# Optimization experiments

Hardware: AMD Instinct MI355X
Metric: run time of the kernel (lower is better)

Reference implementation:

```python
import jax, jax.numpy as jnp
import numpy as np

N_NODES = 50000
N_EDGES = 800000
NUM_FEATURES = 128
HIDDEN = 128
EMBED = 64
OUT_DIM = 1


def setup_inputs() -> dict:
    key = jax.random.key(0)
    ks = jax.random.split(key, 12)
    x = jax.random.normal(ks[0], (N_NODES, NUM_FEATURES), dtype=jnp.float32)
    edge_index = jax.random.randint(ks[1], (2, N_EDGES), 0, N_NODES, dtype=jnp.int64)

    def glorot(k, fan_in, fan_out):
        s = jnp.sqrt(6.0 / (fan_in + fan_out)).astype(jnp.float32)
        return jax.random.uniform(k, (fan_in, fan_out), jnp.float32, -s, s)

    return {
        "x": x,
        "edge_index": edge_index,
        "W1": glorot(ks[2], NUM_FEATURES, HIDDEN),
        "b1": jnp.zeros((HIDDEN,), jnp.float32),
        "Wh": glorot(ks[3], HIDDEN, HIDDEN),
        "bh": jnp.zeros((HIDDEN,), jnp.float32),
        "W2": glorot(ks[4], HIDDEN, EMBED),
        "b2": jnp.zeros((EMBED,), jnp.float32),
        "Wout": glorot(ks[5], EMBED, OUT_DIM),
        "bout": jnp.zeros((OUT_DIM,), jnp.float32),
    }


def _gcn_norm(edge_index, num_nodes):
    # Add self-loops, compute symmetric normalization deg^{-1/2} A_hat deg^{-1/2}
    loop = jnp.arange(num_nodes, dtype=edge_index.dtype)
    src = jnp.concatenate([edge_index[0], loop])
    dst = jnp.concatenate([edge_index[1], loop])
    deg = jax.ops.segment_sum(jnp.ones_like(dst, dtype=jnp.float32), dst,
                              num_segments=num_nodes)
    dis = jnp.where(deg > 0, jax.lax.rsqrt(jnp.maximum(deg, 1.0)), 0.0)
    norm = dis[src] * dis[dst]  # [E+N]
    return src, dst, norm


def _gcn_conv(h, W, b, src, dst, norm, num_nodes):
    h = h @ W  # linear transform first (PyG GCNConv)
    msg = h[src] * norm[:, None]  # gather + scale
    return jax.ops.segment_sum(msg, dst, num_segments=num_nodes) + b


def reference(x, edge_index, W1, b1, Wh, bh, W2, b2, Wout, bout):
    n = x.shape[0]
    src, dst, norm = _gcn_norm(edge_index, n)
    h = jax.nn.relu(_gcn_conv(x, W1, b1, src, dst, norm, n))  # dropout p=0 -> identity
    h = jax.nn.relu(_gcn_conv(h, Wh, bh, src, dst, norm, n))
    h = _gcn_conv(h, W2, b2, src, dst, norm, n)
    out = h @ Wout + bout
    return (out, h)
```

## Files before the change

### kernel.cpp

```cpp
#include <hip/hip_runtime.h>
#include <hip/hip_bf16.h>


#define N_NODES 50000
#define N_EDGES 800000
#define NBUCK 196
#define GB 196
#define EPB 4096

typedef __attribute__((ext_vector_type(8))) short short8;
typedef __attribute__((ext_vector_type(4))) float f32x4;

static __device__ __forceinline__ unsigned short f2bf(float f) {
    __hip_bfloat16 h = __float2bfloat16(f);
    return *reinterpret_cast<unsigned short*>(&h);
}
static __device__ __forceinline__ float bf2f(unsigned short u) {
    return __uint_as_float(((unsigned)u) << 16);
}


__global__ __launch_bounds__(256) void hist_kernel(const int* __restrict__ dstv,
                                                   int* __restrict__ H, int nE) {
    __shared__ int h[NBUCK];
    for (int i = threadIdx.x; i < NBUCK; i += 256) h[i] = 0;
    __syncthreads();
    int base = blockIdx.x * EPB;
#pragma unroll
    for (int i = 0; i < EPB / 256; ++i) {
        int e = base + i * 256 + threadIdx.x;
        if (e < nE) atomicAdd(&h[dstv[e] >> 8], 1);
    }
    __syncthreads();
    for (int i = threadIdx.x; i < NBUCK; i += 256)
        H[i * GB + blockIdx.x] = h[i];
}

__global__ __launch_bounds__(256) void scan1_kernel(int* __restrict__ H,
                                                    int* __restrict__ bsum) {
    __shared__ int s[256];
    int t = threadIdx.x;
    int k = blockIdx.x;
    int v = (t < GB) ? H[k * GB + t] : 0;
    s[t] = v;
    __syncthreads();
    for (int off = 1; off < 256; off <<= 1) {
        int u = (t >= off) ? s[t - off] : 0;
        __syncthreads();
        s[t] += u;
        __syncthreads();
    }
    if (t < GB) H[k * GB + t] = s[t] - v;
    if (t == 255) bsum[k] = s[255];
}

__global__ __launch_bounds__(256) void scan2_kernel(const int* __restrict__ bsum,
                                                    int* __restrict__ bstart,
                                                    int* __restrict__ rowoff_last) {
    __shared__ int s[256];
    int t = threadIdx.x;
    int v = (t < NBUCK) ? bsum[t] : 0;
    s[t] = v;
    __syncthreads();
    for (int off = 1; off < 256; off <<= 1) {
        int u = (t >= off) ? s[t - off] : 0;
        __syncthreads();
        s[t] += u;
        __syncthreads();
    }
    if (t < NBUCK) bstart[t] = s[t] - v;
    if (t == 0) {
        bstart[NBUCK] = N_EDGES;
        *rowoff_last = N_EDGES;
    }
}

__global__ __launch_bounds__(256) void partition_kernel(const int* __restrict__ srcv,
                                                        const int* __restrict__ dstv,
                                                        const int* __restrict__ H,
                                                        const int* __restrict__ bstart,
                                                        unsigned int* __restrict__ P, int nE) {
    __shared__ int cur[NBUCK];
    for (int i = threadIdx.x; i < NBUCK; i += 256)
        cur[i] = bstart[i] + H[i * GB + blockIdx.x];
    __syncthreads();
    int base = blockIdx.x * EPB;
#pragma unroll
    for (int i = 0; i < EPB / 256; ++i) {
        int e = base + i * 256 + threadIdx.x;
        if (e < nE) {
            int d = dstv[e];
            unsigned int pk = (unsigned int)srcv[e] | ((unsigned int)(d & 255) << 16);
            int pos = atomicAdd(&cur[d >> 8], 1);
            P[pos] = pk;
        }
    }
}

__global__ __launch_bounds__(256) void bucket_csr_kernel(const unsigned int* __restrict__ P,
                                                         const int* __restrict__ bstart,
                                                         int* __restrict__ rowoff,
                                                         float* __restrict__ dis,
                                                         int* __restrict__ csr_src, int n) {
    __shared__ int cnt[256];
    __shared__ int s[256];
    __shared__ int cur[256];
    int t = threadIdx.x;
    int k = blockIdx.x;
    int ebeg = bstart[k], eend = bstart[k + 1];
    cnt[t] = 0;
    __syncthreads();
    for (int e = ebeg + t; e < eend; e += 256)
        atomicAdd(&cnt[(P[e] >> 16) & 255], 1);
    __syncthreads();
    int myc = cnt[t];
    s[t] = myc;
    __syncthreads();
    for (int off = 1; off < 256; off <<= 1) {
        int v = (t >= off) ? s[t - off] : 0;
        __syncthreads();
        s[t] += v;
        __syncthreads();
    }
    int excl = s[t] - myc;
    int node = (k << 8) + t;
    if (node < n) {
        rowoff[node] = ebeg + excl;
        dis[node] = rsqrtf((float)(myc + 1));
    }
    cur[t] = ebeg + excl;
    __syncthreads();
    for (int e = ebeg + t; e < eend; e += 256) {
        unsigned int p = P[e];
        int pos = atomicAdd(&cur[(p >> 16) & 255], 1);
        csr_src[pos] = (int)(p & 0xFFFFu);
    }
}

__global__ __launch_bounds__(256) void wprep_all_kernel(
    const float* __restrict__ W1, const float* __restrict__ Wh, const float* __restrict__ W2,
    unsigned short* __restrict__ W1hi, unsigned short* __restrict__ W1lo,
    unsigned short* __restrict__ Whhi, unsigned short* __restrict__ Whlo,
    unsigned short* __restrict__ W2hi, unsigned short* __restrict__ W2lo) {
    int t = blockIdx.x * 256 + threadIdx.x;
    const float* W;
    unsigned short *Hi, *Lo;
    int nout, lt;
    if (t < 16384)      { W = W1; Hi = W1hi; Lo = W1lo; nout = 128; lt = t; }
    else if (t < 32768) { W = Wh; Hi = Whhi; Lo = Whlo; nout = 128; lt = t - 16384; }
    else if (t < 40960) { W = W2; Hi = W2hi; Lo = W2lo; nout = 64;  lt = t - 32768; }
    else return;
    int col = lt % nout, k = lt / nout;
    float v = W[lt];
    unsigned short hi = f2bf(v);
    unsigned short lo = f2bf(v - bf2f(hi));
    Hi[(size_t)col * 128 + k] = hi;
    Lo[(size_t)col * 128 + k] = lo;
}

template <int NOUT>
__global__ __launch_bounds__(256) void gemm_mfma_kernel(
    const float* __restrict__ A,
    const unsigned short* __restrict__ Wthi,
    const unsigned short* __restrict__ Wtlo,
    const float* __restrict__ scale,
    unsigned short* __restrict__ C, int M) {
    constexpr int LDK = 136;
    __shared__ unsigned short sAhi[64 * LDK];
    __shared__ unsigned short sAlo[64 * LDK];

    int tid = threadIdx.x;
    int w = tid >> 6, lane = tid & 63;
    int quad = lane >> 4, m = lane & 15;
    int Rbase = blockIdx.x * 64;
    int Cbase = blockIdx.y * 64;
    int r0 = (w & 1) * 32, c0 = (w >> 1) * 32;

    short8 bh[4][2], bl[4][2];
#pragma unroll
    for (int ks = 0; ks < 4; ++ks)
#pragma unroll
        for (int g = 0; g < 2; ++g) {
            size_t off = (size_t)(Cbase + c0 + g * 16 + m) * 128 + ks * 32 + quad * 8;
            bh[ks][g] = *(const short8*)(Wthi + off);
            bl[ks][g] = *(const short8*)(Wtlo + off);
        }

    for (int i = tid; i < 64 * 32; i += 256) {
        int r = i >> 5, c4 = i & 31;
        int row = Rbase + r;
        float4 v = make_float4(0.f, 0.f, 0.f, 0.f);
        if (row < M) v = ((const float4*)(A + (size_t)row * 128))[c4];
        ushort4 hi, lo;
        hi.x = f2bf(v.x); lo.x = f2bf(v.x - bf2f(hi.x));
        hi.y = f2bf(v.y); lo.y = f2bf(v.y - bf2f(hi.y));
        hi.z = f2bf(v.z); lo.z = f2bf(v.z - bf2f(hi.z));
        hi.w = f2bf(v.w); lo.w = f2bf(v.w - bf2f(hi.w));
        *(ushort4*)(sAhi + r * LDK + c4 * 4) = hi;
        *(ushort4*)(sAlo + r * LDK + c4 * 4) = lo;
    }
    __syncthreads();

    f32x4 z = {0.f, 0.f, 0.f, 0.f};
    f32x4 acc00 = z, acc01 = z, acc10 = z, acc11 = z;

#pragma unroll
    for (int ks = 0; ks < 4; ++ks) {
        int kof = ks * 32 + quad * 8;
        short8 ah0 = *(const short8*)(sAhi + (r0 + m) * LDK + kof);
        short8 ah1 = *(const short8*)(sAhi + (r0 + 16 + m) * LDK + kof);
        short8 al0 = *(const short8*)(sAlo + (r0 + m) * LDK + kof);
        short8 al1 = *(const short8*)(sAlo + (r0 + 16 + m) * LDK + kof);
        acc00 = __builtin_amdgcn_mfma_f32_16x16x32_bf16(ah0, bh[ks][0], acc00, 0, 0, 0);
        acc01 = __builtin_amdgcn_mfma_f32_16x16x32_bf16(ah0, bh[ks][1], acc01, 0, 0, 0);
        acc10 = __builtin_amdgcn_mfma_f32_16x16x32_bf16(ah1, bh[ks][0], acc10, 0, 0, 0);
        acc11 = __builtin_amdgcn_mfma_f32_16x16x32_bf16(ah1, bh[ks][1], acc11, 0, 0, 0);
        acc00 = __builtin_amdgcn_mfma_f32_16x16x32_bf16(ah0, bl[ks][0], acc00, 0, 0, 0);
        acc01 = __builtin_amdgcn_mfma_f32_16x16x32_bf16(ah0, bl[ks][1], acc01, 0, 0, 0);
        acc10 = __builtin_amdgcn_mfma_f32_16x16x32_bf16(ah1, bl[ks][0], acc10, 0, 0, 0);
        acc11 = __builtin_amdgcn_mfma_f32_16x16x32_bf16(ah1, bl[ks][1], acc11, 0, 0, 0);
        acc00 = __builtin_amdgcn_mfma_f32_16x16x32_bf16(al0, bh[ks][0], acc00, 0, 0, 0);
        acc01 = __builtin_amdgcn_mfma_f32_16x16x32_bf16(al0, bh[ks][1], acc01, 0, 0, 0);
        acc10 = __builtin_amdgcn_mfma_f32_16x16x32_bf16(al1, bh[ks][0], acc10, 0, 0, 0);
        acc11 = __builtin_amdgcn_mfma_f32_16x16x32_bf16(al1, bh[ks][1], acc11, 0, 0, 0);
    }

#pragma unroll
    for (int reg = 0; reg < 4; ++reg) {
        int row0g = Rbase + r0 + quad * 4 + reg;
        if (row0g < M) {
            float sc = scale[row0g];
            C[(size_t)row0g * NOUT + Cbase + c0 + m]      = f2bf(acc00[reg] * sc);
            C[(size_t)row0g * NOUT + Cbase + c0 + 16 + m] = f2bf(acc01[reg] * sc);
        }
        int row1g = row0g + 16;
        if (row1g < M) {
            float sc = scale[row1g];
            C[(size_t)row1g * NOUT + Cbase + c0 + m]      = f2bf(acc10[reg] * sc);
            C[(size_t)row1g * NOUT + Cbase + c0 + 16 + m] = f2bf(acc11[reg] * sc);
        }
    }
}

__global__ __launch_bounds__(256) void aggregate128_kernel(
    const int* __restrict__ rowoff, const int* __restrict__ csr_src,
    const float* __restrict__ dis, const unsigned short* __restrict__ tp,
    const float* __restrict__ bias, float* __restrict__ hout, int n) {
    int wid = (blockIdx.x * 256 + threadIdx.x) >> 6;
    int lane = threadIdx.x & 63;
    int h = lane >> 5, lc = lane & 31;
    int n0 = wid * 2;
    if (n0 >= n) return;
    int n1 = n0 + 1;
    bool has1 = (n1 < n);

    float a0[4] = {0.f, 0.f, 0.f, 0.f};
    float a1[4] = {0.f, 0.f, 0.f, 0.f};

#define ROW128(node) (*((const ushort4*)(tp + (size_t)(node) * 128) + lc))
#define ACC(a, u) { a[0] += bf2f(u.x); a[1] += bf2f(u.y); a[2] += bf2f(u.z); a[3] += bf2f(u.w); }

    if (h == 0) { ushort4 u = ROW128(n0); ACC(a0, u); }
    else if (has1) { ushort4 u = ROW128(n1); ACC(a1, u); }

    int mid = rowoff[n0 + 1];
    int i0 = rowoff[n0] + h;
    int i1 = mid + h;
    int end1 = has1 ? rowoff[n1 + 1] : mid;

    while (i0 + 6 < mid && i1 + 6 < end1) {
        int p0 = csr_src[i0], p1 = csr_src[i0 + 2], p2 = csr_src[i0 + 4], p3 = csr_src[i0 + 6];
        int q0 = csr_src[i1], q1 = csr_src[i1 + 2], q2 = csr_src[i1 + 4], q3 = csr_src[i1 + 6];
        ushort4 u0 = ROW128(p0), u1 = ROW128(p1), u2 = ROW128(p2), u3 = ROW128(p3);
        ushort4 v0 = ROW128(q0), v1 = ROW128(q1), v2 = ROW128(q2), v3 = ROW128(q3);
        ACC(a0, u0); ACC(a0, u1); ACC(a0, u2); ACC(a0, u3);
        ACC(a1, v0); ACC(a1, v1); ACC(a1, v2); ACC(a1, v3);
        i0 += 8; i1 += 8;
    }
    while (i0 + 2 < mid && i1 + 2 < end1) {
        int p0 = csr_src[i0], p1 = csr_src[i0 + 2];
        int q0 = csr_src[i1], q1 = csr_src[i1 + 2];
        ushort4 u0 = ROW128(p0), u1 = ROW128(p1);
        ushort4 v0 = ROW128(q0), v1 = ROW128(q1);
        ACC(a0, u0); ACC(a0, u1);
        ACC(a1, v0); ACC(a1, v1);
        i0 += 4; i1 += 4;
    }
    for (; i0 + 2 < mid; i0 += 4) {
        int p0 = csr_src[i0], p1 = csr_src[i0 + 2];
        ushort4 u0 = ROW128(p0), u1 = ROW128(p1);
        ACC(a0, u0); ACC(a0, u1);
    }
    for (; i0 < mid; i0 += 2) { ushort4 u = ROW128(csr_src[i0]); ACC(a0, u); }
    for (; i1 + 2 < end1; i1 += 4) {
        int q0 = csr_src[i1], q1 = csr_src[i1 + 2];
        ushort4 v0 = ROW128(q0), v1 = ROW128(q1);
        ACC(a1, v0); ACC(a1, v1);
    }
    for (; i1 < end1; i1 += 2) { ushort4 v = ROW128(csr_src[i1]); ACC(a1, v); }
#undef ROW128
#undef ACC

#pragma unroll
    for (int j = 0; j < 4; ++j) {
        a0[j] += __shfl_xor(a0[j], 32);
        a1[j] += __shfl_xor(a1[j], 32);
    }

    float4 b = ((const float4*)bias)[lc];
    if (h == 0) {
        float dd = dis[n0];
        float4 r;
        r.x = fmaxf(a0[0] * dd + b.x, 0.f);
        r.y = fmaxf(a0[1] * dd + b.y, 0.f);
        r.z = fmaxf(a0[2] * dd + b.z, 0.f);
        r.w = fmaxf(a0[3] * dd + b.w, 0.f);
        ((float4*)(hout + (size_t)n0 * 128))[lc] = r;
    } else if (has1) {
        float dd = dis[n1];
        float4 r;
        r.x = fmaxf(a1[0] * dd + b.x, 0.f);
        r.y = fmaxf(a1[1] * dd + b.y, 0.f);
        r.z = fmaxf(a1[2] * dd + b.z, 0.f);
        r.w = fmaxf(a1[3] * dd + b.w, 0.f);
        ((float4*)(hout + (size_t)n1 * 128))[lc] = r;
    }
}

__global__ __launch_bounds__(256) void aggregate64_head_kernel(
    const int* __restrict__ rowoff, const int* __restrict__ csr_src,
    const float* __restrict__ dis, const unsigned short* __restrict__ tp,
    const float* __restrict__ bias, const float* __restrict__ Wout,
    const float* __restrict__ bout, float* __restrict__ hout,
    float* __restrict__ out, int n) {
    int wid = (blockIdx.x * 256 + threadIdx.x) >> 6;
    int lane = threadIdx.x & 63;
    int h = lane >> 5, lc = lane & 31;
    int n0 = wid * 2;
    if (n0 >= n) return;
    int n1 = n0 + 1;
    bool has1 = (n1 < n);

    float a0[2] = {0.f, 0.f};
    float a1[2] = {0.f, 0.f};

#define ROW64(node) (*((const ushort2*)(tp + (size_t)(node) * 64) + lc))
#define ACC2(a, u) { a[0] += bf2f(u.x); a[1] += bf2f(u.y); }

    if (h == 0) { ushort2 u = ROW64(n0); ACC2(a0, u); }
    else if (has1) { ushort2 u = ROW64(n1); ACC2(a1, u); }

    int mid = rowoff[n0 + 1];
    int i0 = rowoff[n0] + h;
    int i1 = mid + h;
    int end1 = has1 ? rowoff[n1 + 1] : mid;

    while (i0 + 6 < mid && i1 + 6 < end1) {
        int p0 = csr_src[i0], p1 = csr_src[i0 + 2], p2 = csr_src[i0 + 4], p3 = csr_src[i0 + 6];
        int q0 = csr_src[i1], q1 = csr_src[i1 + 2], q2 = csr_src[i1 + 4], q3 = csr_src[i1 + 6];
        ushort2 u0 = ROW64(p0), u1 = ROW64(p1), u2 = ROW64(p2), u3 = ROW64(p3);
        ushort2 v0 = ROW64(q0), v1 = ROW64(q1), v2 = ROW64(q2), v3 = ROW64(q3);
        ACC2(a0, u0); ACC2(a0, u1); ACC2(a0, u2); ACC2(a0, u3);
        ACC2(a1, v0); ACC2(a1, v1); ACC2(a1, v2); ACC2(a1, v3);
        i0 += 8; i1 += 8;
    }
    while (i0 + 2 < mid && i1 + 2 < end1) {
        int p0 = csr_src[i0], p1 = csr_src[i0 + 2];
        int q0 = csr_src[i1], q1 = csr_src[i1 + 2];
        ushort2 u0 = ROW64(p0), u1 = ROW64(p1);
        ushort2 v0 = ROW64(q0), v1 = ROW64(q1);
        ACC2(a0, u0); ACC2(a0, u1);
        ACC2(a1, v0); ACC2(a1, v1);
        i0 += 4; i1 += 4;
    }
    for (; i0 < mid; i0 += 2) { ushort2 u = ROW64(csr_src[i0]); ACC2(a0, u); }
    for (; i1 < end1; i1 += 2) { ushort2 v = ROW64(csr_src[i1]); ACC2(a1, v); }
#undef ROW64
#undef ACC2

#pragma unroll
    for (int j = 0; j < 2; ++j) {
        a0[j] += __shfl_xor(a0[j], 32);
        a1[j] += __shfl_xor(a1[j], 32);
    }

    int node = h ? n1 : n0;
    float* ap = h ? a1 : a0;
    bool valid = (h == 0) || has1;
    float2 hv = make_float2(0.f, 0.f);
    if (valid) {
        float dd = dis[node];
        float2 b = ((const float2*)bias)[lc];
        hv.x = ap[0] * dd + b.x;
        hv.y = ap[1] * dd + b.y;
        ((float2*)(hout + (size_t)node * 64))[lc] = hv;
    }
    float2 wv = ((const float2*)Wout)[lc];
    float p = valid ? (hv.x * wv.x + hv.y * wv.y) : 0.f;
#pragma unroll
    for (int off = 16; off > 0; off >>= 1) p += __shfl_down(p, off);
    if (lc == 0 && valid) out[node] = p + bout[0];
}

extern "C" void kernel_launch(void* const* d_in, const int* in_sizes, int n_in,
                              void* d_out, int out_size, void* d_ws, size_t ws_size,
                              hipStream_t stream) {
    const float* x    = (const float*)d_in[0];
    const int*   ei   = (const int*)d_in[1];
    const float* W1   = (const float*)d_in[2];
    const float* b1   = (const float*)d_in[3];
    const float* Wh   = (const float*)d_in[4];
    const float* bh   = (const float*)d_in[5];
    const float* W2   = (const float*)d_in[6];
    const float* b2   = (const float*)d_in[7];
    const float* Wout = (const float*)d_in[8];
    const float* bout = (const float*)d_in[9];

    const int N = N_NODES;
    const int E = N_EDGES;
    const int* srcv = ei;
    const int* dstv = ei + E;

    float* out  = (float*)d_out;
    float* hout = (float*)d_out + N;

    char* ws = (char*)d_ws;
    int*   H       = (int*)ws;                          ws += sizeof(int) * NBUCK * GB;
    int*   bsum    = (int*)ws;                          ws += sizeof(int) * NBUCK;
    int*   bstart  = (int*)ws;                          ws += sizeof(int) * (NBUCK + 1);
    int*   rowoff  = (int*)ws;                          ws += sizeof(int) * (N + 1);
    unsigned int* P = (unsigned int*)ws;                ws += sizeof(unsigned int) * E;
    int*   csr_src = (int*)ws;                          ws += sizeof(int) * E;
    float* dis     = (float*)ws;                        ws += sizeof(float) * N;
    unsigned short* W1thi = (unsigned short*)ws;        ws += sizeof(unsigned short) * 128 * 128;
    unsigned short* W1tlo = (unsigned short*)ws;        ws += sizeof(unsigned short) * 128 * 128;
    unsigned short* Whthi = (unsigned short*)ws;        ws += sizeof(unsigned short) * 128 * 128;
    unsigned short* Whtlo = (unsigned short*)ws;        ws += sizeof(unsigned short) * 128 * 128;
    unsigned short* W2thi = (unsigned short*)ws;        ws += sizeof(unsigned short) * 64 * 128;
    unsigned short* W2tlo = (unsigned short*)ws;        ws += sizeof(unsigned short) * 64 * 128;
    unsigned short* bufT  = (unsigned short*)ws;        ws += sizeof(unsigned short) * (size_t)N * 128;
    float* bufH    = (float*)ws;

    wprep_all_kernel<<<160, 256, 0, stream>>>(W1, Wh, W2, W1thi, W1tlo, Whthi, Whtlo, W2thi, W2tlo);

    hist_kernel<<<GB, 256, 0, stream>>>(dstv, H, E);
    scan1_kernel<<<NBUCK, 256, 0, stream>>>(H, bsum);
    scan2_kernel<<<1, 256, 0, stream>>>(bsum, bstart, rowoff + N);
    partition_kernel<<<GB, 256, 0, stream>>>(srcv, dstv, H, bstart, P, E);
    bucket_csr_kernel<<<NBUCK, 256, 0, stream>>>(P, bstart, rowoff, dis, csr_src, N);

    const int aggBlocks = ((N + 1) / 2 * 64 + 255) / 256;
    const int gemmRows = (N + 63) / 64;

    gemm_mfma_kernel<128><<<dim3(gemmRows, 2), 256, 0, stream>>>(x, W1thi, W1tlo, dis, bufT, N);
    aggregate128_kernel<<<aggBlocks, 256, 0, stream>>>(rowoff, csr_src, dis, bufT, b1, bufH, N);

    gemm_mfma_kernel<128><<<dim3(gemmRows, 2), 256, 0, stream>>>(bufH, Whthi, Whtlo, dis, bufT, N);
    aggregate128_kernel<<<aggBlocks, 256, 0, stream>>>(rowoff, csr_src, dis, bufT, bh, bufH, N);

    gemm_mfma_kernel<64><<<dim3(gemmRows, 1), 256, 0, stream>>>(bufH, W2thi, W2tlo, dis, bufT, N);
    aggregate64_head_kernel<<<aggBlocks, 256, 0, stream>>>(
        rowoff, csr_src, dis, bufT, b2, Wout, bout, hout, out, N);
}
```

Before: 295.0 us.

## Fuse weight prep into histogram, merge scans via ticket, single-pass GEMM over columns

Weight bf16 hi/lo splitting is folded into the histogram kernel, and the two scan kernels become one, where the last-finishing block (chosen by an atomic ticket) performs the bucket-level scan. The 128-wide GEMMs now run one block per 64-row tile and loop over both 64-column halves, so the A tile is loaded and split into bf16 once instead of twice. This removes two kernel launches and halves A reads and conversion work. In exchange there is less grid parallelism, more serial work per block, and a reliance on threadfence/atomic ordering for the last-block scan.

```diff
diff --git a/kernel.cpp b/kernel.cpp
--- a/kernel.cpp
+++ b/kernel.cpp
@@ -20,8 +20,29 @@
 }
 
 
-__global__ __launch_bounds__(256) void hist_kernel(const int* __restrict__ dstv,
-                                                   int* __restrict__ H, int nE) {
+__global__ __launch_bounds__(256) void hist_wprep_kernel(
+    const int* __restrict__ dstv, int* __restrict__ H, int nE, int* __restrict__ ticket,
+    const float* __restrict__ W1, const float* __restrict__ Wh, const float* __restrict__ W2,
+    unsigned short* __restrict__ W1hi, unsigned short* __restrict__ W1lo,
+    unsigned short* __restrict__ Whhi, unsigned short* __restrict__ Whlo,
+    unsigned short* __restrict__ W2hi, unsigned short* __restrict__ W2lo) {
+    int gt = blockIdx.x * 256 + threadIdx.x;
+    if (gt == 0) *ticket = 0;
+    if (gt < 40960) {
+        const float* W;
+        unsigned short *Hi, *Lo;
+        int nout, lt;
+        if (gt < 16384)      { W = W1; Hi = W1hi; Lo = W1lo; nout = 128; lt = gt; }
+        else if (gt < 32768) { W = Wh; Hi = Whhi; Lo = Whlo; nout = 128; lt = gt - 16384; }
+        else                 { W = W2; Hi = W2hi; Lo = W2lo; nout = 64;  lt = gt - 32768; }
+        int col = lt % nout, k = lt / nout;
+        float v = W[lt];
+        unsigned short hi = f2bf(v);
+        unsigned short lo = f2bf(v - bf2f(hi));
+        Hi[(size_t)col * 128 + k] = hi;
+        Lo[(size_t)col * 128 + k] = lo;
+    }
+
     __shared__ int h[NBUCK];
     for (int i = threadIdx.x; i < NBUCK; i += 256) h[i] = 0;
     __syncthreads();
@@ -36,9 +57,13 @@
         H[i * GB + blockIdx.x] = h[i];
 }
 
-__global__ __launch_bounds__(256) void scan1_kernel(int* __restrict__ H,
-                                                    int* __restrict__ bsum) {
+__global__ __launch_bounds__(256) void scan_kernel(int* __restrict__ H,
+                                                   int* __restrict__ bsum,
+                                                   int* __restrict__ bstart,
+                                                   int* __restrict__ rowoff_last,
+                                                   int* __restrict__ ticket) {
     __shared__ int s[256];
+    __shared__ int lastFlag;
     int t = threadIdx.x;
     int k = blockIdx.x;
     int v = (t < GB) ? H[k * GB + t] : 0;
@@ -51,16 +76,17 @@
         __syncthreads();
     }
     if (t < GB) H[k * GB + t] = s[t] - v;
-    if (t == 255) bsum[k] = s[255];
-}
-
-__global__ __launch_bounds__(256) void scan2_kernel(const int* __restrict__ bsum,
-                                                    int* __restrict__ bstart,
-                                                    int* __restrict__ rowoff_last) {
-    __shared__ int s[256];
-    int t = threadIdx.x;
-    int v = (t < NBUCK) ? bsum[t] : 0;
-    s[t] = v;
+    if (t == 255) {
+        bsum[k] = s[255];
+        __threadfence();
+        int tk = atomicAdd(ticket, 1);
+        lastFlag = (tk == NBUCK - 1);
+    }
+    __syncthreads();
+    if (!lastFlag) return;
+    __threadfence();
+    int v2 = (t < NBUCK) ? bsum[t] : 0;
+    s[t] = v2;
     __syncthreads();
     for (int off = 1; off < 256; off <<= 1) {
         int u = (t >= off) ? s[t - off] : 0;
@@ -68,7 +94,7 @@
         s[t] += u;
         __syncthreads();
     }
-    if (t < NBUCK) bstart[t] = s[t] - v;
+    if (t < NBUCK) bstart[t] = s[t] - v2;
     if (t == 0) {
         bstart[NBUCK] = N_EDGES;
         *rowoff_last = N_EDGES;
@@ -137,27 +163,6 @@
     }
 }
 
-__global__ __launch_bounds__(256) void wprep_all_kernel(
-    const float* __restrict__ W1, const float* __restrict__ Wh, const float* __restrict__ W2,
-    unsigned short* __restrict__ W1hi, unsigned short* __restrict__ W1lo,
-    unsigned short* __restrict__ Whhi, unsigned short* __restrict__ Whlo,
-    unsigned short* __restrict__ W2hi, unsigned short* __restrict__ W2lo) {
-    int t = blockIdx.x * 256 + threadIdx.x;
-    const float* W;
-    unsigned short *Hi, *Lo;
-    int nout, lt;
-    if (t < 16384)      { W = W1; Hi = W1hi; Lo = W1lo; nout = 128; lt = t; }
-    else if (t < 32768) { W = Wh; Hi = Whhi; Lo = Whlo; nout = 128; lt = t - 16384; }
-    else if (t < 40960) { W = W2; Hi = W2hi; Lo = W2lo; nout = 64;  lt = t - 32768; }
-    else return;
-    int col = lt % nout, k = lt / nout;
-    float v = W[lt];
-    unsigned short hi = f2bf(v);
-    unsigned short lo = f2bf(v - bf2f(hi));
-    Hi[(size_t)col * 128 + k] = hi;
-    Lo[(size_t)col * 128 + k] = lo;
-}
-
 template <int NOUT>
 __global__ __launch_bounds__(256) void gemm_mfma_kernel(
     const float* __restrict__ A,
@@ -173,18 +178,64 @@
     int w = tid >> 6, lane = tid & 63;
     int quad = lane >> 4, m = lane & 15;
     int Rbase = blockIdx.x * 64;
-    int Cbase = blockIdx.y * 64;
     int r0 = (w & 1) * 32, c0 = (w >> 1) * 32;
 
     short8 bh[4][2], bl[4][2];
-#pragma unroll
-    for (int ks = 0; ks < 4; ++ks)
-#pragma unroll
-        for (int g = 0; g < 2; ++g) {
-            size_t off = (size_t)(Cbase + c0 + g * 16 + m) * 128 + ks * 32 + quad * 8;
-            bh[ks][g] = *(const short8*)(Wthi + off);
-            bl[ks][g] = *(const short8*)(Wtlo + off);
+    f32x4 acc00, acc01, acc10, acc11;
+
+    auto loadB = [&](int CB) {
+#pragma unroll
+        for (int ks = 0; ks < 4; ++ks)
+#pragma unroll
+            for (int g = 0; g < 2; ++g) {
+                size_t off = (size_t)(CB + c0 + g * 16 + m) * 128 + ks * 32 + quad * 8;
+                bh[ks][g] = *(const short8*)(Wthi + off);
+                bl[ks][g] = *(const short8*)(Wtlo + off);
+            }
+    };
+
+    auto kloop = [&]() {
+#pragma unroll
+        for (int ks = 0; ks < 4; ++ks) {
+            int kof = ks * 32 + quad * 8;
+            short8 ah0 = *(const short8*)(sAhi + (r0 + m) * LDK + kof);
+            short8 ah1 = *(const short8*)(sAhi + (r0 + 16 + m) * LDK + kof);
+            short8 al0 = *(const short8*)(sAlo + (r0 + m) * LDK + kof);
+            short8 al1 = *(const short8*)(sAlo + (r0 + 16 + m) * LDK + kof);
+            acc00 = __builtin_amdgcn_mfma_f32_16x16x32_bf16(ah0, bh[ks][0], acc00, 0, 0, 0);
+            acc01 = __builtin_amdgcn_mfma_f32_16x16x32_bf16(ah0, bh[ks][1], acc01, 0, 0, 0);
+            acc10 = __builtin_amdgcn_mfma_f32_16x16x32_bf16(ah1, bh[ks][0], acc10, 0, 0, 0);
+            acc11 = __builtin_amdgcn_mfma_f32_16x16x32_bf16(ah1, bh[ks][1], acc11, 0, 0, 0);
+            acc00 = __builtin_amdgcn_mfma_f32_16x16x32_bf16(ah0, bl[ks][0], acc00, 0, 0, 0);
+            acc01 = __builtin_amdgcn_mfma_f32_16x16x32_bf16(ah0, bl[ks][1], acc01, 0, 0, 0);
+            acc10 = __builtin_amdgcn_mfma_f32_16x16x32_bf16(ah1, bl[ks][0], acc10, 0, 0, 0);
+            acc11 = __builtin_amdgcn_mfma_f32_16x16x32_bf16(ah1, bl[ks][1], acc11, 0, 0, 0);
+            acc00 = __builtin_amdgcn_mfma_f32_16x16x32_bf16(al0, bh[ks][0], acc00, 0, 0, 0);
+            acc01 = __builtin_amdgcn_mfma_f32_16x16x32_bf16(al0, bh[ks][1], acc01, 0, 0, 0);
+            acc10 = __builtin_amdgcn_mfma_f32_16x16x32_bf16(al1, bh[ks][0], acc10, 0, 0, 0);
+            acc11 = __builtin_amdgcn_mfma_f32_16x16x32_bf16(al1, bh[ks][1], acc11, 0, 0, 0);
         }
+    };
+
+    auto writeC = [&](int CB) {
+#pragma unroll
+        for (int reg = 0; reg < 4; ++reg) {
+            int row0g = Rbase + r0 + quad * 4 + reg;
+            if (row0g < M) {
+                float sc = scale[row0g];
+                C[(size_t)row0g * NOUT + CB + c0 + m]      = f2bf(acc00[reg] * sc);
+                C[(size_t)row0g * NOUT + CB + c0 + 16 + m] = f2bf(acc01[reg] * sc);
+            }
+            int row1g = row0g + 16;
+            if (row1g < M) {
+                float sc = scale[row1g];
+                C[(size_t)row1g * NOUT + CB + c0 + m]      = f2bf(acc10[reg] * sc);
+                C[(size_t)row1g * NOUT + CB + c0 + 16 + m] = f2bf(acc11[reg] * sc);
+            }
+        }
+    };
+
+    loadB(0);
 
     for (int i = tid; i < 64 * 32; i += 256) {
         int r = i >> 5, c4 = i & 31;
@@ -202,43 +253,14 @@
     __syncthreads();
 
     f32x4 z = {0.f, 0.f, 0.f, 0.f};
-    f32x4 acc00 = z, acc01 = z, acc10 = z, acc11 = z;
-
-#pragma unroll
-    for (int ks = 0; ks < 4; ++ks) {
-        int kof = ks * 32 + quad * 8;
-        short8 ah0 = *(const short8*)(sAhi + (r0 + m) * LDK + kof);
-        short8 ah1 = *(const short8*)(sAhi + (r0 + 16 + m) * LDK + kof);
-        short8 al0 = *(const short8*)(sAlo + (r0 + m) * LDK + kof);
-        short8 al1 = *(const short8*)(sAlo + (r0 + 16 + m) * LDK + kof);
-        acc00 = __builtin_amdgcn_mfma_f32_16x16x32_bf16(ah0, bh[ks][0], acc00, 0, 0, 0);
-        acc01 = __builtin_amdgcn_mfma_f32_16x16x32_bf16(ah0, bh[ks][1], acc01, 0, 0, 0);
-        acc10 = __builtin_amdgcn_mfma_f32_16x16x32_bf16(ah1, bh[ks][0], acc10, 0, 0, 0);
-        acc11 = __builtin_amdgcn_mfma_f32_16x16x32_bf16(ah1, bh[ks][1], acc11, 0, 0, 0);
-        acc00 = __builtin_amdgcn_mfma_f32_16x16x32_bf16(ah0, bl[ks][0], acc00, 0, 0, 0);
-        acc01 = __builtin_amdgcn_mfma_f32_16x16x32_bf16(ah0, bl[ks][1], acc01, 0, 0, 0);
-        acc10 = __builtin_amdgcn_mfma_f32_16x16x32_bf16(ah1, bl[ks][0], acc10, 0, 0, 0);
-        acc11 = __builtin_amdgcn_mfma_f32_16x16x32_bf16(ah1, bl[ks][1], acc11, 0, 0, 0);
-        acc00 = __builtin_amdgcn_mfma_f32_16x16x32_bf16(al0, bh[ks][0], acc00, 0, 0, 0);
-        acc01 = __builtin_amdgcn_mfma_f32_16x16x32_bf16(al0, bh[ks][1], acc01, 0, 0, 0);
-        acc10 = __builtin_amdgcn_mfma_f32_16x16x32_bf16(al1, bh[ks][0], acc10, 0, 0, 0);
-        acc11 = __builtin_amdgcn_mfma_f32_16x16x32_bf16(al1, bh[ks][1], acc11, 0, 0, 0);
-    }
-
-#pragma unroll
-    for (int reg = 0; reg < 4; ++reg) {
-        int row0g = Rbase + r0 + quad * 4 + reg;
-        if (row0g < M) {
-            float sc = scale[row0g];
-            C[(size_t)row0g * NOUT + Cbase + c0 + m]      = f2bf(acc00[reg] * sc);
-            C[(size_t)row0g * NOUT + Cbase + c0 + 16 + m] = f2bf(acc01[reg] * sc);
-        }
-        int row1g = row0g + 16;
-        if (row1g < M) {
-            float sc = scale[row1g];
-            C[(size_t)row1g * NOUT + Cbase + c0 + m]      = f2bf(acc10[reg] * sc);
-            C[(size_t)row1g * NOUT + Cbase + c0 + 16 + m] = f2bf(acc11[reg] * sc);
-        }
+    acc00 = z; acc01 = z; acc10 = z; acc11 = z;
+    kloop();
+    if constexpr (NOUT == 128) loadB(64);
+    writeC(0);
+    if constexpr (NOUT == 128) {
+        acc00 = z; acc01 = z; acc10 = z; acc11 = z;
+        kloop();
+        writeC(64);
     }
 }
 
@@ -428,6 +450,7 @@
     int*   H       = (int*)ws;                          ws += sizeof(int) * NBUCK * GB;
     int*   bsum    = (int*)ws;                          ws += sizeof(int) * NBUCK;
     int*   bstart  = (int*)ws;                          ws += sizeof(int) * (NBUCK + 1);
+    int*   ticket  = (int*)ws;                          ws += sizeof(int) * 4;
     int*   rowoff  = (int*)ws;                          ws += sizeof(int) * (N + 1);
     unsigned int* P = (unsigned int*)ws;                ws += sizeof(unsigned int) * E;
     int*   csr_src = (int*)ws;                          ws += sizeof(int) * E;
@@ -441,24 +464,22 @@
     unsigned short* bufT  = (unsigned short*)ws;        ws += sizeof(unsigned short) * (size_t)N * 128;
     float* bufH    = (float*)ws;
 
-    wprep_all_kernel<<<160, 256, 0, stream>>>(W1, Wh, W2, W1thi, W1tlo, Whthi, Whtlo, W2thi, W2tlo);
-
-    hist_kernel<<<GB, 256, 0, stream>>>(dstv, H, E);
-    scan1_kernel<<<NBUCK, 256, 0, stream>>>(H, bsum);
-    scan2_kernel<<<1, 256, 0, stream>>>(bsum, bstart, rowoff + N);
+    hist_wprep_kernel<<<GB, 256, 0, stream>>>(dstv, H, E, ticket,
+                                              W1, Wh, W2, W1thi, W1tlo, Whthi, Whtlo, W2thi, W2tlo);
+    scan_kernel<<<NBUCK, 256, 0, stream>>>(H, bsum, bstart, rowoff + N, ticket);
     partition_kernel<<<GB, 256, 0, stream>>>(srcv, dstv, H, bstart, P, E);
     bucket_csr_kernel<<<NBUCK, 256, 0, stream>>>(P, bstart, rowoff, dis, csr_src, N);
 
     const int aggBlocks = ((N + 1) / 2 * 64 + 255) / 256;
     const int gemmRows = (N + 63) / 64;
 
-    gemm_mfma_kernel<128><<<dim3(gemmRows, 2), 256, 0, stream>>>(x, W1thi, W1tlo, dis, bufT, N);
+    gemm_mfma_kernel<128><<<gemmRows, 256, 0, stream>>>(x, W1thi, W1tlo, dis, bufT, N);
     aggregate128_kernel<<<aggBlocks, 256, 0, stream>>>(rowoff, csr_src, dis, bufT, b1, bufH, N);
 
-    gemm_mfma_kernel<128><<<dim3(gemmRows, 2), 256, 0, stream>>>(bufH, Whthi, Whtlo, dis, bufT, N);
+    gemm_mfma_kernel<128><<<gemmRows, 256, 0, stream>>>(bufH, Whthi, Whtlo, dis, bufT, N);
     aggregate128_kernel<<<aggBlocks, 256, 0, stream>>>(rowoff, csr_src, dis, bufT, bh, bufH, N);
 
-    gemm_mfma_kernel<64><<<dim3(gemmRows, 1), 256, 0, stream>>>(bufH, W2thi, W2tlo, dis, bufT, N);
+    gemm_mfma_kernel<64><<<gemmRows, 256, 0, stream>>>(bufH, W2thi, W2tlo, dis, bufT, N);
     aggregate64_head_kernel<<<aggBlocks, 256, 0, stream>>>(
         rowoff, csr_src, dis, bufT, b2, Wout, bout, hout, out, N);
 }
```

After: 304.0 us. 1.03x slower.
